# Optimization experiments

Hardware: AMD Instinct MI355X
Metric: run time of the kernel (lower is better)

## Reference

```python
import jax, jax.numpy as jnp
import numpy as np

N, D = 8192, 64


def setup_inputs() -> dict:
    key = jax.random.key(0)
    k1, k2, k3 = jax.random.split(key, 3)
    X = jax.random.normal(k1, (N, D), dtype=jnp.float32)
    target = jax.random.normal(k2, (N,), dtype=jnp.float32)
    params = jax.random.uniform(k3, (D,), dtype=jnp.float32)  # positive ARD weights
    return {"X": X, "target": target, "params": params}


def reference(X, target, params):
    # ARD-RBF kernel: k(x, y) = exp(-sum(params * (x - y)^2))
    # = exp(-||xs - ys||^2) with xs = x * sqrt(params)
    Xs = X * jnp.sqrt(params)  # [N, D]
    sq = jnp.sum(Xs * Xs, axis=-1)  # [N]
    d2 = jnp.maximum(sq[:, None] + sq[None, :] - 2.0 * (Xs @ Xs.T), 0.0)  # [N, N]
    K = jnp.exp(-d2)
    # torch version initializes K = eye(N) and never overwrites the diagonal
    n = X.shape[0]
    K = K.at[jnp.arange(n), jnp.arange(n)].set(1.0)
    K_target = jnp.outer(target, target)  # [N, N]
    kta = jnp.sum(K * K_target) / (n * jnp.sqrt(jnp.sum(K * K)))
    return -kta
```

## Files before the change

kernel.cpp:

```cpp
#include <hip/hip_runtime.h>
#include <hip/hip_bf16.h>

#define NROWS 8192
#define DIM 64
#define NT 64
#define NTRI (NT * (NT + 1) / 2)

typedef __attribute__((ext_vector_type(8))) short short8;
typedef __attribute__((ext_vector_type(4))) float f32x4;

static constexpr float LOG2E = 1.4426950408889634f;

#if defined(__has_builtin) && __has_builtin(__builtin_amdgcn_exp2f)
#define EXP2F(x) __builtin_amdgcn_exp2f(x)
#else
#define EXP2F(x) exp2f(x)
#endif

__global__ __launch_bounds__(256) void prep_kernel(const float* __restrict__ X,
                                                   const float* __restrict__ params,
                                                   float* __restrict__ Lsq,
                                                   short* __restrict__ Xp) {
    int tid  = threadIdx.x;
    int wave = tid >> 6, lane = tid & 63;
    int r8 = lane >> 3, c = lane & 7;
    int row = blockIdx.x * 32 + wave * 8 + r8;

    const float* xr = X + row * DIM + c * 8;
    float4 x0 = *(const float4*)xr;
    float4 x1 = *(const float4*)(xr + 4);
    float4 p0 = *(const float4*)(params + c * 8);
    float4 p1 = *(const float4*)(params + c * 8 + 4);

    float v[8];
    v[0] = x0.x * sqrtf(p0.x); v[1] = x0.y * sqrtf(p0.y);
    v[2] = x0.z * sqrtf(p0.z); v[3] = x0.w * sqrtf(p0.w);
    v[4] = x1.x * sqrtf(p1.x); v[5] = x1.y * sqrtf(p1.y);
    v[6] = x1.z * sqrtf(p1.z); v[7] = x1.w * sqrtf(p1.w);

    short8 h;
    float s = 0.f;
    #pragma unroll
    for (int i = 0; i < 8; ++i) {
        __hip_bfloat16 b = __float2bfloat16(v[i]);
        union { __hip_bfloat16 bb; short ss; } u; u.bb = b;
        h[i] = u.ss;
        float bf = __bfloat162float(b);
        s += bf * bf;
    }

    int panel = row >> 4, pr = row & 15;
    ((short8*)Xp)[panel * 128 + c * 16 + pr] = h;

    #pragma unroll
    for (int m = 1; m < 8; m <<= 1) s += __shfl_xor(s, m, 64);
    if (c == 0) Lsq[row] = LOG2E * s;
}

__global__ __launch_bounds__(256) void kta_main(const short* __restrict__ Xp,
                                                const float* __restrict__ Lsq,
                                                const float* __restrict__ t,
                                                float2* __restrict__ partial) {
    int k = blockIdx.x;
    int it = (int)((129.0f - sqrtf(16641.0f - 8.0f * (float)k)) * 0.5f);
    if (it > NT - 1) it = NT - 1;
    while ((it * (129 - it)) / 2 > k) --it;
    while (((it + 1) * (128 - it)) / 2 <= k) ++it;
    int jt = it + (k - (it * (129 - it)) / 2);

    int tid  = threadIdx.x;
    int wave = tid >> 6, lane = tid & 63;
    int quad = lane >> 4, l16 = lane & 15;
    int rbase = it * 128 + (wave >> 1) * 64;
    int cbase = jt * 128 + (wave & 1) * 64;

    const short8* Xpv = (const short8*)Xp;
    int pA0 = rbase >> 4, pB0 = cbase >> 4;
    short8 afr[4][2], bfr[4][2];
    #pragma unroll
    for (int rt = 0; rt < 4; ++rt) {
        #pragma unroll
        for (int kc = 0; kc < 2; ++kc) {
            afr[rt][kc] = Xpv[(pA0 + rt) * 128 + (kc * 4 + quad) * 16 + l16];
            bfr[rt][kc] = Xpv[(pB0 + rt) * 128 + (kc * 4 + quad) * 16 + l16];
        }
    }

    f32x4 c[4][4];
    #pragma unroll
    for (int rt = 0; rt < 4; ++rt)
        #pragma unroll
        for (int ct = 0; ct < 4; ++ct)
            c[rt][ct] = (f32x4){0.f, 0.f, 0.f, 0.f};

    #pragma unroll
    for (int rt = 0; rt < 4; ++rt)
        #pragma unroll
        for (int ct = 0; ct < 4; ++ct) {
            c[rt][ct] = __builtin_amdgcn_mfma_f32_16x16x32_bf16(afr[rt][0], bfr[ct][0], c[rt][ct], 0, 0, 0);
            c[rt][ct] = __builtin_amdgcn_mfma_f32_16x16x32_bf16(afr[rt][1], bfr[ct][1], c[rt][ct], 0, 0, 0);
        }

    float LsqR[4][4], tR[4][4];
    #pragma unroll
    for (int rt = 0; rt < 4; ++rt)
        #pragma unroll
        for (int r = 0; r < 4; ++r) {
            int row = rbase + rt * 16 + quad * 4 + r;
            LsqR[rt][r] = Lsq[row];
            tR[rt][r]   = t[row];
        }
    float LsqC[4], tC[4];
    #pragma unroll
    for (int ct = 0; ct < 4; ++ct) {
        int col = cbase + ct * 16 + l16;
        LsqC[ct] = Lsq[col];
        tC[ct]   = t[col];
    }

    bool diagwave = (it == jt) && ((wave >> 1) == (wave & 1));
    int col_l = cbase + l16;

    float s1 = 0.f, s2 = 0.f;
    #pragma unroll
    for (int rt = 0; rt < 4; ++rt)
        #pragma unroll
        for (int r = 0; r < 4; ++r) {
            int row = rbase + rt * 16 + quad * 4 + r;
            float nr = LsqR[rt][r];
            float s1row = 0.f;
            #pragma unroll
            for (int ct = 0; ct < 4; ++ct) {
                float dot = c[rt][ct][r];
                float K = EXP2F(fmaf(dot, 2.0f * LOG2E, -(nr + LsqC[ct])));
                if (diagwave && (row == (col_l + ct * 16)))
                    K = 1.0f;
                s1row = fmaf(K, tC[ct], s1row);
                s2    = fmaf(K, K, s2);
            }
            s1 = fmaf(s1row, tR[rt][r], s1);
        }

    float w = (it == jt) ? 1.0f : 2.0f;
    s1 *= w; s2 *= w;
    #pragma unroll
    for (int m = 32; m > 0; m >>= 1) {
        s1 += __shfl_xor(s1, m, 64);
        s2 += __shfl_xor(s2, m, 64);
    }

    __shared__ float2 red[4];
    if (lane == 0) red[wave] = make_float2(s1, s2);
    __syncthreads();
    if (tid == 0) {
        float2 a = red[0], b = red[1], cc = red[2], d = red[3];
        partial[k] = make_float2(a.x + b.x + cc.x + d.x, a.y + b.y + cc.y + d.y);
    }
}

__global__ __launch_bounds__(256) void finalize_kernel(const float2* __restrict__ partial,
                                                       float* __restrict__ out) {
    float s1 = 0.f, s2 = 0.f;
    for (int i = threadIdx.x; i < NTRI; i += 256) {
        float2 p = partial[i];
        s1 += p.x;
        s2 += p.y;
    }
    #pragma unroll
    for (int m = 32; m > 0; m >>= 1) {
        s1 += __shfl_xor(s1, m, 64);
        s2 += __shfl_xor(s2, m, 64);
    }
    __shared__ float r1[4], r2[4];
    int wave = threadIdx.x >> 6, lane = threadIdx.x & 63;
    if (lane == 0) { r1[wave] = s1; r2[wave] = s2; }
    __syncthreads();
    if (threadIdx.x == 0) {
        float a = r1[0] + r1[1] + r1[2] + r1[3];
        float b = r2[0] + r2[1] + r2[2] + r2[3];
        out[0] = -a / ((float)NROWS * sqrtf(b));
    }
}

extern "C" void kernel_launch(void* const* d_in, const int* in_sizes, int n_in,
                              void* d_out, int out_size, void* d_ws, size_t ws_size,
                              hipStream_t stream) {
    const float* X      = (const float*)d_in[0];
    const float* target = (const float*)d_in[1];
    const float* params = (const float*)d_in[2];
    float* out = (float*)d_out;

    float* ws = (float*)d_ws;
    float2* partial = (float2*)ws;
    float* Lsq = ws + 8192;
    short* Xp  = (short*)(ws + 16384);

    prep_kernel<<<NROWS / 32, 256, 0, stream>>>(X, params, Lsq, Xp);
    kta_main<<<NTRI, 256, 0, stream>>>(Xp, Lsq, target, partial);
    finalize_kernel<<<1, 256, 0, stream>>>(partial, out);
}
```

Before: 76.03 us.

## Fuse finalize into main kernel via last-block atomic and restructure MFMA epilogue

```diff
diff --git a/kernel.cpp b/kernel.cpp
--- a/kernel.cpp
+++ b/kernel.cpp
@@ -20,7 +20,10 @@
 __global__ __launch_bounds__(256) void prep_kernel(const float* __restrict__ X,
                                                    const float* __restrict__ params,
                                                    float* __restrict__ Lsq,
-                                                   short* __restrict__ Xp) {
+                                                   short* __restrict__ Xp,
+                                                   unsigned* __restrict__ counter) {
+    if (blockIdx.x == 0 && threadIdx.x == 0) *counter = 0u;
+
     int tid  = threadIdx.x;
     int wave = tid >> 6, lane = tid & 63;
     int r8 = lane >> 3, c = lane & 7;
@@ -57,10 +60,12 @@
     if (c == 0) Lsq[row] = LOG2E * s;
 }
 
-__global__ __launch_bounds__(256) void kta_main(const short* __restrict__ Xp,
-                                                const float* __restrict__ Lsq,
-                                                const float* __restrict__ t,
-                                                float2* __restrict__ partial) {
+__global__ __launch_bounds__(256, 4) void kta_main(const short* __restrict__ Xp,
+                                                   const float* __restrict__ Lsq,
+                                                   const float* __restrict__ t,
+                                                   float2* __restrict__ partial,
+                                                   unsigned* __restrict__ counter,
+                                                   float* __restrict__ out) {
     int k = blockIdx.x;
     int it = (int)((129.0f - sqrtf(16641.0f - 8.0f * (float)k)) * 0.5f);
     if (it > NT - 1) it = NT - 1;
@@ -86,30 +91,6 @@
         }
     }
 
-    f32x4 c[4][4];
-    #pragma unroll
-    for (int rt = 0; rt < 4; ++rt)
-        #pragma unroll
-        for (int ct = 0; ct < 4; ++ct)
-            c[rt][ct] = (f32x4){0.f, 0.f, 0.f, 0.f};
-
-    #pragma unroll
-    for (int rt = 0; rt < 4; ++rt)
-        #pragma unroll
-        for (int ct = 0; ct < 4; ++ct) {
-            c[rt][ct] = __builtin_amdgcn_mfma_f32_16x16x32_bf16(afr[rt][0], bfr[ct][0], c[rt][ct], 0, 0, 0);
-            c[rt][ct] = __builtin_amdgcn_mfma_f32_16x16x32_bf16(afr[rt][1], bfr[ct][1], c[rt][ct], 0, 0, 0);
-        }
-
-    float LsqR[4][4], tR[4][4];
-    #pragma unroll
-    for (int rt = 0; rt < 4; ++rt)
-        #pragma unroll
-        for (int r = 0; r < 4; ++r) {
-            int row = rbase + rt * 16 + quad * 4 + r;
-            LsqR[rt][r] = Lsq[row];
-            tR[rt][r]   = t[row];
-        }
     float LsqC[4], tC[4];
     #pragma unroll
     for (int ct = 0; ct < 4; ++ct) {
@@ -119,28 +100,47 @@
     }
 
     bool diagwave = (it == jt) && ((wave >> 1) == (wave & 1));
-    int col_l = cbase + l16;
-
-    float s1 = 0.f, s2 = 0.f;
-    #pragma unroll
-    for (int rt = 0; rt < 4; ++rt)
+
+    float s1 = 0.f, s2a = 0.f, s2b = 0.f;
+
+    auto run = [&](int DIAG) {
         #pragma unroll
-        for (int r = 0; r < 4; ++r) {
-            int row = rbase + rt * 16 + quad * 4 + r;
-            float nr = LsqR[rt][r];
-            float s1row = 0.f;
+        for (int rt = 0; rt < 4; ++rt) {
+            float nr4[4], tr4[4];
+            #pragma unroll
+            for (int r = 0; r < 4; ++r) {
+                int row = rbase + rt * 16 + quad * 4 + r;
+                nr4[r] = Lsq[row];
+                tr4[r] = t[row];
+            }
+            f32x4 cc[4];
             #pragma unroll
             for (int ct = 0; ct < 4; ++ct) {
-                float dot = c[rt][ct][r];
-                float K = EXP2F(fmaf(dot, 2.0f * LOG2E, -(nr + LsqC[ct])));
-                if (diagwave && (row == (col_l + ct * 16)))
-                    K = 1.0f;
-                s1row = fmaf(K, tC[ct], s1row);
-                s2    = fmaf(K, K, s2);
+                cc[ct] = (f32x4){0.f, 0.f, 0.f, 0.f};
+                cc[ct] = __builtin_amdgcn_mfma_f32_16x16x32_bf16(afr[rt][0], bfr[ct][0], cc[ct], 0, 0, 0);
+                cc[ct] = __builtin_amdgcn_mfma_f32_16x16x32_bf16(afr[rt][1], bfr[ct][1], cc[ct], 0, 0, 0);
             }
-            s1 = fmaf(s1row, tR[rt][r], s1);
-        }
-
+            #pragma unroll
+            for (int r = 0; r < 4; ++r) {
+                float nr = nr4[r];
+                float s1row = 0.f;
+                #pragma unroll
+                for (int ct = 0; ct < 4; ++ct) {
+                    float dot = cc[ct][r];
+                    float K = EXP2F(fmaf(dot, 2.0f * LOG2E, -(nr + LsqC[ct])));
+                    if (DIAG && (rt == ct) && ((quad * 4 + r) == l16))
+                        K = 1.0f;
+                    s1row = fmaf(K, tC[ct], s1row);
+                    if (ct & 2) s2b = fmaf(K, K, s2b);
+                    else        s2a = fmaf(K, K, s2a);
+                }
+                s1 = fmaf(s1row, tr4[r], s1);
+            }
+        }
+    };
+    if (diagwave) run(1); else run(0);
+
+    float s2 = s2a + s2b;
     float w = (it == jt) ? 1.0f : 2.0f;
     s1 *= w; s2 *= w;
     #pragma unroll
@@ -150,35 +150,41 @@
     }
 
     __shared__ float2 red[4];
+    __shared__ int isLast;
     if (lane == 0) red[wave] = make_float2(s1, s2);
     __syncthreads();
     if (tid == 0) {
         float2 a = red[0], b = red[1], cc = red[2], d = red[3];
         partial[k] = make_float2(a.x + b.x + cc.x + d.x, a.y + b.y + cc.y + d.y);
-    }
-}
-
-__global__ __launch_bounds__(256) void finalize_kernel(const float2* __restrict__ partial,
-                                                       float* __restrict__ out) {
-    float s1 = 0.f, s2 = 0.f;
-    for (int i = threadIdx.x; i < NTRI; i += 256) {
-        float2 p = partial[i];
-        s1 += p.x;
-        s2 += p.y;
-    }
-    #pragma unroll
-    for (int m = 32; m > 0; m >>= 1) {
-        s1 += __shfl_xor(s1, m, 64);
-        s2 += __shfl_xor(s2, m, 64);
-    }
-    __shared__ float r1[4], r2[4];
-    int wave = threadIdx.x >> 6, lane = threadIdx.x & 63;
-    if (lane == 0) { r1[wave] = s1; r2[wave] = s2; }
+        __threadfence();
+        unsigned prev = atomicAdd(counter, 1u);
+        isLast = (prev == (unsigned)(NTRI - 1));
+    }
     __syncthreads();
-    if (threadIdx.x == 0) {
-        float a = r1[0] + r1[1] + r1[2] + r1[3];
-        float b = r2[0] + r2[1] + r2[2] + r2[3];
-        out[0] = -a / ((float)NROWS * sqrtf(b));
+
+    if (isLast) {
+        __threadfence();
+        float f1 = 0.f, f2 = 0.f;
+        const unsigned long long* pu = (const unsigned long long*)partial;
+        for (int i = tid; i < NTRI; i += 256) {
+            unsigned long long v = __hip_atomic_load(pu + i, __ATOMIC_RELAXED,
+                                                     __HIP_MEMORY_SCOPE_AGENT);
+            union { unsigned long long u; float2 f; } cv; cv.u = v;
+            f1 += cv.f.x;
+            f2 += cv.f.y;
+        }
+        #pragma unroll
+        for (int m = 32; m > 0; m >>= 1) {
+            f1 += __shfl_xor(f1, m, 64);
+            f2 += __shfl_xor(f2, m, 64);
+        }
+        if (lane == 0) red[wave] = make_float2(f1, f2);
+        __syncthreads();
+        if (tid == 0) {
+            float a = red[0].x + red[1].x + red[2].x + red[3].x;
+            float b = red[0].y + red[1].y + red[2].y + red[3].y;
+            out[0] = -a / ((float)NROWS * sqrtf(b));
+        }
     }
 }
 
@@ -192,10 +198,10 @@
 
     float* ws = (float*)d_ws;
     float2* partial = (float2*)ws;
+    unsigned* counter = (unsigned*)(ws + 7168);
     float* Lsq = ws + 8192;
     short* Xp  = (short*)(ws + 16384);
 
-    prep_kernel<<<NROWS / 32, 256, 0, stream>>>(X, params, Lsq, Xp);
-    kta_main<<<NTRI, 256, 0, stream>>>(Xp, Lsq, target, partial);
-    finalize_kernel<<<1, 256, 0, stream>>>(partial, out);
+    prep_kernel<<<NROWS / 32, 256, 0, stream>>>(X, params, Lsq, Xp, counter);
+    kta_main<<<NTRI, 256, 0, stream>>>(Xp, Lsq, target, partial, counter, out);
 }
```

Result: slower. 103.8 us (+36.5%).
